# Kernel tuning notes

Hardware: AMD Instinct MI355X
Metric: run time of the kernel (lower is better)

## Reference

```python
import jax, jax.numpy as jnp
import numpy as np

N_STATES = 32
N_CAMP = 64
DAYS = 365
BATCH = 128
BASIS = 1e-10


def setup_inputs() -> dict:
    key = jax.random.key(0)
    k1, k2, k3 = jax.random.split(key, 3)
    S = N_STATES
    adstock = jax.random.uniform(k1, (BATCH, N_CAMP, DAYS), dtype=jnp.float32)
    mu = jax.random.uniform(k2, ((S - 1) * (S - 1),), dtype=jnp.float32)
    beta = jax.random.uniform(k3, (N_CAMP * (S - 1) * (S - 1),), dtype=jnp.float32)
    return {"adstock": adstock, "mu": mu, "beta": beta}


def _transition(adstock, mu, beta):
    # adstock: [B, C, D]; time T = D - 1 (first day dropped, as in adstock[:, :, 1:])
    S = N_STATES
    B, C, D = adstock.shape
    T = D - 1
    # call() passes -mu into make_transition_matrix
    mu_m = jnp.reshape(-mu, (1, 1, S - 1, S - 1))
    beta_m = jnp.reshape(beta, (C, S - 1, S - 1))
    # tensordot(adstock[b, :, 1:], beta, [0, 0]) for every b -> einsum over camp axis
    O_beta = jnp.einsum('bct,cij->btij', adstock[:, :, 1:], beta_m)  # [B,T,S-1,S-1]
    num = jnp.exp(O_beta + mu_m)
    den = 1.0 + jnp.sum(num, axis=-1, keepdims=True)
    Q_div = num / den                          # [B,T,S-1,S-1] off-diagonal probs
    Q_same = 1.0 - jnp.sum(Q_div, axis=-1)     # [B,T,S-1]    stay probability
    # The TF diag-set loop places, for row i of Q_div: columns j<i stay at j,
    # columns j>=i shift to j+1, and Q_same goes on column i (insert-diagonal).
    i = jnp.arange(S - 1)[:, None]             # [S-1,1]
    j = jnp.arange(S)[None, :]                 # [1,S]
    idx = jnp.clip(jnp.where(j < i, j, j - 1), 0, S - 2)  # [S-1,S]
    gathered = jnp.take_along_axis(Q_div, jnp.broadcast_to(idx, (B, T, S - 1, S)), axis=-1)
    Q_temp = jnp.where(j == i, Q_same[..., None], gathered)  # [B,T,S-1,S]
    # Absorbing last row: basis everywhere, mass 1-(S-1)*basis on last state.
    last = jnp.full((B, T, 1, S), BASIS, dtype=adstock.dtype)
    last = last.at[..., -1].set(1.0 - (S - 1) * BASIS)
    Q = jnp.concatenate([Q_temp, last], axis=2)  # [B,T,S,S]
    return jnp.maximum(Q, BASIS)


def reference(adstock, mu, beta):
    return _transition(adstock, mu, beta)
```

## Files before the change

### kernel.cpp

```cpp
#include <hip/hip_runtime.h>
#include <cstdint>
#include <cstddef>

#define Bb 128
#define Cc 64
#define Dd 365
#define Tt 364
#define Ss 32
#define SM1 31
#define NIJ 961
#define BASISF 1e-10f
#define NTILES 728
#define NBLK 256

typedef _Float16 f16x8 __attribute__((ext_vector_type(8)));
typedef _Float16 f16x4 __attribute__((ext_vector_type(4)));
typedef float f32x4 __attribute__((ext_vector_type(4)));

__global__ void prep_kernel(const float* __restrict__ mu,
                            const float* __restrict__ beta,
                            _Float16* __restrict__ B2,
                            float* __restrict__ emu_perm) {
    int idx = blockIdx.x * blockDim.x + threadIdx.x;
    int m = idx >> 6, c = idx & 63;
    int nq = m >> 8, rem = m & 255, qp = rem >> 6, p = (rem >> 4) & 3, v = rem & 15;
    int i = nq * 8 + qp * 2 + (v >> 3);
    int j = 4 * (v & 7) + p;
    float val = (i < SM1 && j < SM1) ? beta[c * NIJ + i * SM1 + j] : 0.0f;
    B2[((size_t)(c >> 3) * 1024 + m) * 8 + (c & 7)] = (_Float16)val;
    if (idx < 1024) {
        int m2 = idx;
        int nq2 = m2 >> 8, rem2 = m2 & 255, qp2 = rem2 >> 6;
        int p2 = (rem2 >> 4) & 3, v2 = rem2 & 15;
        int i2 = nq2 * 8 + qp2 * 2 + (v2 >> 3);
        int j2 = 4 * (v2 & 7) + p2;
        emu_perm[m2] = (i2 < SM1 && j2 < SM1) ? __expf(-mu[i2 * SM1 + j2]) : 1.0f;
    }
}

template <int CTRL>
__device__ __forceinline__ float dpp_mov(float x) {
    union { float f; int i; } u, v;
    u.f = x;
    v.i = __builtin_amdgcn_update_dpp(0, u.i, CTRL, 0xf, 0xf, true);
    return v.f;
}
template <int CTRL>
__device__ __forceinline__ float dpp_add(float s) { return s + dpp_mov<CTRL>(s); }

__global__ __launch_bounds__(1024, 1)
void transition_persist_kernel(const float* __restrict__ adstock,
                               const _Float16* __restrict__ B2,
                               const float* __restrict__ emu_perm,
                               float* __restrict__ out)
{
    const int tid  = threadIdx.x;
    const int lane = tid & 63;
    const int w    = tid >> 6;
    const int je   = lane & 15;
    const int grp  = lane >> 4;
    const int mh   = w >> 2;
    const int nq   = w & 3;
    const int a     = je & 7;
    const int ihalf = je >> 3;
    const int j0    = 4 * a;

    __shared__ _Float16 Blds[65536];
    __shared__ __align__(16) _Float16 Alds[64][72];

    #pragma unroll
    for (int s = 0; s < 8; ++s) {
        const int o8 = s * 8192 + tid * 8;
        *reinterpret_cast<f16x8*>(&Blds[o8]) =
            *reinterpret_cast<const f16x8*>(B2 + o8);
    }

    float emu[4][4];
    #pragma unroll
    for (int qp = 0; qp < 4; ++qp)
        #pragma unroll
        for (int p = 0; p < 4; ++p)
            emu[qp][p] = emu_perm[nq * 256 + qp * 64 + p * 16 + je];

    const float m3 = (a == 7) ? 0.0f : 1.0f;

    const int tb = (NTILES * blockIdx.x) / NBLK;
    const int te = (NTILES * (blockIdx.x + 1)) / NBLK;

    const int m_s = tid >> 4;
    const int c0  = (tid & 15) * 4;

    float av0, av1, av2, av3;
    {
        const int bt = tb * 64 + m_s;
        const int b = bt / Tt, t = bt - b * Tt;
        av0 = adstock[((size_t)b * Cc + c0 + 0) * Dd + 1 + t];
        av1 = adstock[((size_t)b * Cc + c0 + 1) * Dd + 1 + t];
        av2 = adstock[((size_t)b * Cc + c0 + 2) * Dd + 1 + t];
        av3 = adstock[((size_t)b * Cc + c0 + 3) * Dd + 1 + t];
    }

    for (int tile = tb; tile < te; ++tile) {
        __syncthreads();
        {
            f16x4 pk = {(_Float16)av0, (_Float16)av1, (_Float16)av2, (_Float16)av3};
            *reinterpret_cast<f16x4*>(&Alds[m_s][c0]) = pk;
        }
        __syncthreads();

        if (tile + 1 < te) {
            const int bt = (tile + 1) * 64 + m_s;
            const int b = bt / Tt, t = bt - b * Tt;
            av0 = adstock[((size_t)b * Cc + c0 + 0) * Dd + 1 + t];
            av1 = adstock[((size_t)b * Cc + c0 + 1) * Dd + 1 + t];
            av2 = adstock[((size_t)b * Cc + c0 + 2) * Dd + 1 + t];
            av3 = adstock[((size_t)b * Cc + c0 + 3) * Dd + 1 + t];
        }

        const f16x8 a0 = *reinterpret_cast<const f16x8*>(&Alds[mh * 16 + je][grp * 8]);
        const f16x8 a1 = *reinterpret_cast<const f16x8*>(&Alds[mh * 16 + je][32 + grp * 8]);

        const int bt0 = tile * 64 + mh * 16;

        #pragma unroll
        for (int qp = 0; qp < 4; ++qp) {
            const int colb = nq * 256 + qp * 64 + je;
            f16x8 Bf[8];
            #pragma unroll
            for (int p = 0; p < 4; ++p) {
                Bf[2 * p]     = *reinterpret_cast<const f16x8*>(
                    &Blds[((0 * 4 + grp) * 1024 + colb + p * 16) * 8]);
                Bf[2 * p + 1] = *reinterpret_cast<const f16x8*>(
                    &Blds[((1 * 4 + grp) * 1024 + colb + p * 16) * 8]);
            }

            f32x4 acc[4];
            #pragma unroll
            for (int p = 0; p < 4; ++p) {
                f32x4 z = {0.f, 0.f, 0.f, 0.f};
                f32x4 t0 = __builtin_amdgcn_mfma_f32_16x16x32_f16(a0, Bf[2 * p], z, 0, 0, 0);
                acc[p] = __builtin_amdgcn_mfma_f32_16x16x32_f16(a1, Bf[2 * p + 1], t0, 0, 0, 0);
            }

            const int i_lane = nq * 8 + 2 * qp + ihalf;
            const size_t obase = (size_t)(bt0 + grp * 4) * 1024
                               + (size_t)i_lane * 32 + j0;

            #pragma unroll
            for (int r = 0; r < 4; ++r) {
                float np[4];
                #pragma unroll
                for (int p = 0; p < 4; ++p) np[p] = __expf(acc[p][r]) * emu[qp][p];

                float s = np[0] + np[1] + fmaf(np[3], m3, np[2]);
                s = dpp_add<0xB1>(s);
                s = dpp_add<0x4E>(s);
                float t1 = dpp_mov<0x124>(s);
                float t2 = dpp_mov<0x12C>(s);
                s += (je & 4) ? t1 : t2;
                const float inv = __builtin_amdgcn_rcpf(1.0f + s);

                const float sh0 = dpp_mov<0x111>(np[3]);
                const float prev[4] = {sh0, np[0], np[1], np[2]};

                float v[4];
                #pragma unroll
                for (int p = 0; p < 4; ++p) {
                    const int j = j0 + p;
                    float x = (j < i_lane) ? np[p] * inv
                            : ((j == i_lane) ? inv : prev[p] * inv);
                    v[p] = fmaxf(x, BASISF);
                }
                if (nq == 3 && qp == 3) {
                    const bool ab = (i_lane == SM1);
                    v[0] = ab ? BASISF : v[0];
                    v[1] = ab ? BASISF : v[1];
                    v[2] = ab ? BASISF : v[2];
                    v[3] = ab ? ((a == 7) ? (1.0f - SM1 * BASISF) : BASISF) : v[3];
                }
                f32x4 vv = {v[0], v[1], v[2], v[3]};
                *reinterpret_cast<f32x4*>(out + obase + (size_t)r * 1024) = vv;
            }
        }
    }
}

__global__ __launch_bounds__(256, 4)
void transition_fallback_kernel(const float* __restrict__ adstock,
                                const float* __restrict__ beta,
                                const float* __restrict__ mu,
                                float* __restrict__ out) {
    const int b  = blockIdx.x;
    const int t0 = blockIdx.y * 16;
    const int tid = threadIdx.x;

    __shared__ float adT[Cc][16];
    __shared__ float num_lds[8][964];

    for (int k = tid; k < Cc * 16; k += 256) {
        int c = k >> 4, tt = k & 15, t = t0 + tt;
        adT[c][tt] = (t < Tt) ? adstock[(size_t)b * (Cc * Dd) + c * Dd + 1 + t] : 0.0f;
    }
    __syncthreads();

    const int ij0 = tid * 4;
    const bool active = (ij0 < 964);
    float acc[16][4];
    #pragma unroll
    for (int tt = 0; tt < 16; ++tt) { acc[tt][0]=0;acc[tt][1]=0;acc[tt][2]=0;acc[tt][3]=0; }

    if (active) {
        for (int c = 0; c < Cc; ++c) {
            const float* bsrc = beta + (size_t)c * NIJ;
            float w0 = (ij0+0<NIJ)?bsrc[ij0+0]:0.f, w1 = (ij0+1<NIJ)?bsrc[ij0+1]:0.f;
            float w2 = (ij0+2<NIJ)?bsrc[ij0+2]:0.f, w3 = (ij0+3<NIJ)?bsrc[ij0+3]:0.f;
            #pragma unroll
            for (int tt = 0; tt < 16; ++tt) {
                float av = adT[c][tt];
                acc[tt][0] = fmaf(av, w0, acc[tt][0]);
                acc[tt][1] = fmaf(av, w1, acc[tt][1]);
                acc[tt][2] = fmaf(av, w2, acc[tt][2]);
                acc[tt][3] = fmaf(av, w3, acc[tt][3]);
            }
        }
    }
    float m0=0,m1=0,m2=0,m3=0;
    if (active) {
        m0 = (ij0+0<NIJ)?mu[ij0+0]:0.f; m1 = (ij0+1<NIJ)?mu[ij0+1]:0.f;
        m2 = (ij0+2<NIJ)?mu[ij0+2]:0.f; m3 = (ij0+3<NIJ)?mu[ij0+3]:0.f;
    }
    const int q8 = tid >> 5, irow = tid & 31;
    #pragma unroll
    for (int half = 0; half < 2; ++half) {
        if (active) {
            #pragma unroll
            for (int q = 0; q < 8; ++q) {
                const int tt = half * 8 + q;
                num_lds[q][ij0+0] = __expf(acc[tt][0] - m0);
                num_lds[q][ij0+1] = __expf(acc[tt][1] - m1);
                num_lds[q][ij0+2] = __expf(acc[tt][2] - m2);
                num_lds[q][ij0+3] = __expf(acc[tt][3] - m3);
            }
        }
        __syncthreads();
        const int t = t0 + half * 8 + q8;
        if (t < Tt) {
            float* op = out + (((size_t)b * Tt + t) * Ss + irow) * Ss;
            if (irow < SM1) {
                float row[SM1]; float den = 1.0f;
                #pragma unroll
                for (int j = 0; j < SM1; ++j) { row[j] = num_lds[q8][irow*SM1+j]; den += row[j]; }
                const float inv = 1.0f / den;
                #pragma unroll
                for (int j = 0; j < Ss; ++j) {
                    float vv = (j < irow) ? row[j]*inv : ((j == irow) ? inv
                              : (j-1 < SM1 ? row[j-1]*inv : 0.f));
                    op[j] = fmaxf(vv, BASISF);
                }
            } else {
                #pragma unroll
                for (int j = 0; j < Ss; ++j) op[j] = (j == SM1) ? (1.0f - SM1*BASISF) : BASISF;
            }
        }
        __syncthreads();
    }
}

extern "C" void kernel_launch(void* const* d_in, const int* in_sizes, int n_in,
                              void* d_out, int out_size, void* d_ws, size_t ws_size,
                              hipStream_t stream) {
    const float* adstock = (const float*)d_in[0];
    const float* mu      = (const float*)d_in[1];
    const float* beta    = (const float*)d_in[2];
    float* out = (float*)d_out;

    const size_t need = (size_t)65536 * sizeof(_Float16) + 1024 * sizeof(float);

    if (ws_size >= need) {
        _Float16* B2 = (_Float16*)d_ws;
        float* emu_perm = (float*)((char*)d_ws + (size_t)65536 * sizeof(_Float16));
        prep_kernel<<<(1024 * Cc) / 256, 256, 0, stream>>>(mu, beta, B2, emu_perm);
        transition_persist_kernel<<<NBLK, 1024, 0, stream>>>(adstock, B2, emu_perm, out);
    } else {
        dim3 grid(Bb, (Tt + 15) / 16);
        transition_fallback_kernel<<<grid, 256, 0, stream>>>(adstock, beta, mu, out);
    }
}
```

Measured before the change: 43.56 us.

## Distribute per-wave work units and load A fragments directly from global memory

Replaces the block-level 64-row tile loop, which staged adstock through LDS with two __syncthreads per tile, with independent per-wave work units (16 rows × one i-quarter) split evenly across all waves. Each wave loads its own A fragment straight from global memory and converts it to fp16, which removes the block barriers and lets waves progress independently. The exp(-mu) factors move from registers into LDS to lower register pressure. The trade-off is that each adstock element is now loaded by four waves instead of once, and the global loads are strided with no prefetch overlap.

```diff
diff --git a/kernel.cpp b/kernel.cpp
--- a/kernel.cpp
+++ b/kernel.cpp
@@ -10,11 +10,11 @@
 #define SM1 31
 #define NIJ 961
 #define BASISF 1e-10f
-#define NTILES 728
 #define NBLK 256
+#define NUNITS 11648
+#define NWAVES 4096
 
 typedef _Float16 f16x8 __attribute__((ext_vector_type(8)));
-typedef _Float16 f16x4 __attribute__((ext_vector_type(4)));
 typedef float f32x4 __attribute__((ext_vector_type(4)));
 
 __global__ void prep_kernel(const float* __restrict__ mu,
@@ -23,17 +23,15 @@
                             float* __restrict__ emu_perm) {
     int idx = blockIdx.x * blockDim.x + threadIdx.x;
     int m = idx >> 6, c = idx & 63;
-    int nq = m >> 8, rem = m & 255, qp = rem >> 6, p = (rem >> 4) & 3, v = rem & 15;
-    int i = nq * 8 + qp * 2 + (v >> 3);
-    int j = 4 * (v & 7) + p;
+    int rem = m & 255;
+    int i = (m >> 8) * 8 + (rem >> 6) * 2 + ((rem & 15) >> 3);
+    int j = 4 * (rem & 7) + ((rem >> 4) & 3);
     float val = (i < SM1 && j < SM1) ? beta[c * NIJ + i * SM1 + j] : 0.0f;
     B2[((size_t)(c >> 3) * 1024 + m) * 8 + (c & 7)] = (_Float16)val;
     if (idx < 1024) {
-        int m2 = idx;
-        int nq2 = m2 >> 8, rem2 = m2 & 255, qp2 = rem2 >> 6;
-        int p2 = (rem2 >> 4) & 3, v2 = rem2 & 15;
-        int i2 = nq2 * 8 + qp2 * 2 + (v2 >> 3);
-        int j2 = 4 * (v2 & 7) + p2;
+        int m2 = idx, rem2 = m2 & 255;
+        int i2 = (m2 >> 8) * 8 + (rem2 >> 6) * 2 + ((rem2 & 15) >> 3);
+        int j2 = 4 * (rem2 & 7) + ((rem2 >> 4) & 3);
         emu_perm[m2] = (i2 < SM1 && j2 < SM1) ? __expf(-mu[i2 * SM1 + j2]) : 1.0f;
     }
 }
@@ -59,14 +57,12 @@
     const int w    = tid >> 6;
     const int je   = lane & 15;
     const int grp  = lane >> 4;
-    const int mh   = w >> 2;
-    const int nq   = w & 3;
     const int a     = je & 7;
     const int ihalf = je >> 3;
     const int j0    = 4 * a;
 
     __shared__ _Float16 Blds[65536];
-    __shared__ __align__(16) _Float16 Alds[64][72];
+    __shared__ float emuL[1024];
 
     #pragma unroll
     for (int s = 0; s < 8; ++s) {
@@ -74,53 +70,36 @@
         *reinterpret_cast<f16x8*>(&Blds[o8]) =
             *reinterpret_cast<const f16x8*>(B2 + o8);
     }
-
-    float emu[4][4];
-    #pragma unroll
-    for (int qp = 0; qp < 4; ++qp)
+    emuL[tid] = emu_perm[tid];
+    __syncthreads();
+
+    const float m3 = (a == 7) ? 0.0f : 1.0f;
+
+    const int gw = blockIdx.x * 16 + w;
+    const int ub = (int)(((long)NUNITS * gw) / NWAVES);
+    const int ue = (int)(((long)NUNITS * (gw + 1)) / NWAVES);
+
+    for (int u = ub; u < ue; ++u) {
+        const int chunk = u >> 2;
+        const int nq    = u & 3;
+        const int bt0   = chunk * 16;
+
+        const int bt = bt0 + je;
+        const int b  = bt / Tt, t = bt - b * Tt;
+        const float* abase = adstock + ((size_t)b * Cc) * Dd + 1 + t;
+
+        float a0f[8], a1f[8];
         #pragma unroll
-        for (int p = 0; p < 4; ++p)
-            emu[qp][p] = emu_perm[nq * 256 + qp * 64 + p * 16 + je];
-
-    const float m3 = (a == 7) ? 0.0f : 1.0f;
-
-    const int tb = (NTILES * blockIdx.x) / NBLK;
-    const int te = (NTILES * (blockIdx.x + 1)) / NBLK;
-
-    const int m_s = tid >> 4;
-    const int c0  = (tid & 15) * 4;
-
-    float av0, av1, av2, av3;
-    {
-        const int bt = tb * 64 + m_s;
-        const int b = bt / Tt, t = bt - b * Tt;
-        av0 = adstock[((size_t)b * Cc + c0 + 0) * Dd + 1 + t];
-        av1 = adstock[((size_t)b * Cc + c0 + 1) * Dd + 1 + t];
-        av2 = adstock[((size_t)b * Cc + c0 + 2) * Dd + 1 + t];
-        av3 = adstock[((size_t)b * Cc + c0 + 3) * Dd + 1 + t];
-    }
-
-    for (int tile = tb; tile < te; ++tile) {
-        __syncthreads();
-        {
-            f16x4 pk = {(_Float16)av0, (_Float16)av1, (_Float16)av2, (_Float16)av3};
-            *reinterpret_cast<f16x4*>(&Alds[m_s][c0]) = pk;
-        }
-        __syncthreads();
-
-        if (tile + 1 < te) {
-            const int bt = (tile + 1) * 64 + m_s;
-            const int b = bt / Tt, t = bt - b * Tt;
-            av0 = adstock[((size_t)b * Cc + c0 + 0) * Dd + 1 + t];
-            av1 = adstock[((size_t)b * Cc + c0 + 1) * Dd + 1 + t];
-            av2 = adstock[((size_t)b * Cc + c0 + 2) * Dd + 1 + t];
-            av3 = adstock[((size_t)b * Cc + c0 + 3) * Dd + 1 + t];
-        }
-
-        const f16x8 a0 = *reinterpret_cast<const f16x8*>(&Alds[mh * 16 + je][grp * 8]);
-        const f16x8 a1 = *reinterpret_cast<const f16x8*>(&Alds[mh * 16 + je][32 + grp * 8]);
-
-        const int bt0 = tile * 64 + mh * 16;
+        for (int u8 = 0; u8 < 8; ++u8) {
+            a0f[u8] = abase[(size_t)(grp * 8 + u8) * Dd];
+            a1f[u8] = abase[(size_t)(32 + grp * 8 + u8) * Dd];
+        }
+        f16x8 a0, a1;
+        #pragma unroll
+        for (int u8 = 0; u8 < 8; ++u8) {
+            a0[u8] = (_Float16)a0f[u8];
+            a1[u8] = (_Float16)a1f[u8];
+        }
 
         #pragma unroll
         for (int qp = 0; qp < 4; ++qp) {
@@ -134,6 +113,11 @@
                     &Blds[((1 * 4 + grp) * 1024 + colb + p * 16) * 8]);
             }
 
+            float emq[4];
+            #pragma unroll
+            for (int p = 0; p < 4; ++p)
+                emq[p] = emuL[nq * 256 + qp * 64 + p * 16 + je];
+
             f32x4 acc[4];
             #pragma unroll
             for (int p = 0; p < 4; ++p) {
@@ -150,7 +134,7 @@
             for (int r = 0; r < 4; ++r) {
                 float np[4];
                 #pragma unroll
-                for (int p = 0; p < 4; ++p) np[p] = __expf(acc[p][r]) * emu[qp][p];
+                for (int p = 0; p < 4; ++p) np[p] = __expf(acc[p][r]) * emq[p];
 
                 float s = np[0] + np[1] + fmaf(np[3], m3, np[2]);
                 s = dpp_add<0xB1>(s);
```

Result: slower. 48.35 us (+11.0%).

## Split output columns across block pairs with half-size B in LDS

Applied to the files above, without the earlier changes.

Each 1024-thread block becomes two 512-thread blocks. Each of the pair handles half of the output column groups (i rows) for the same time-tile slot and loads only half of the fp16 beta matrix into LDS. This halves per-block LDS and allows several blocks per CU, aiming for better occupancy and latency hiding than a single huge block. In exchange, each adstock tile is loaded and converted twice, once per column half.

```diff
diff --git a/kernel.cpp b/kernel.cpp
--- a/kernel.cpp
+++ b/kernel.cpp
@@ -10,8 +10,9 @@
 #define SM1 31
 #define NIJ 961
 #define BASISF 1e-10f
-#define NTILES 728
-#define NBLK 256
+#define NT64 728
+#define NSLOT 256
+#define NBLK2 512
 
 typedef _Float16 f16x8 __attribute__((ext_vector_type(8)));
 typedef _Float16 f16x4 __attribute__((ext_vector_type(4)));
@@ -23,17 +24,15 @@
                             float* __restrict__ emu_perm) {
     int idx = blockIdx.x * blockDim.x + threadIdx.x;
     int m = idx >> 6, c = idx & 63;
-    int nq = m >> 8, rem = m & 255, qp = rem >> 6, p = (rem >> 4) & 3, v = rem & 15;
-    int i = nq * 8 + qp * 2 + (v >> 3);
-    int j = 4 * (v & 7) + p;
+    int rem = m & 255;
+    int i = (m >> 8) * 8 + (rem >> 6) * 2 + ((rem & 15) >> 3);
+    int j = 4 * (rem & 7) + ((rem >> 4) & 3);
     float val = (i < SM1 && j < SM1) ? beta[c * NIJ + i * SM1 + j] : 0.0f;
     B2[((size_t)(c >> 3) * 1024 + m) * 8 + (c & 7)] = (_Float16)val;
     if (idx < 1024) {
-        int m2 = idx;
-        int nq2 = m2 >> 8, rem2 = m2 & 255, qp2 = rem2 >> 6;
-        int p2 = (rem2 >> 4) & 3, v2 = rem2 & 15;
-        int i2 = nq2 * 8 + qp2 * 2 + (v2 >> 3);
-        int j2 = 4 * (v2 & 7) + p2;
+        int m2 = idx, rem2 = m2 & 255;
+        int i2 = (m2 >> 8) * 8 + (rem2 >> 6) * 2 + ((rem2 & 15) >> 3);
+        int j2 = 4 * (rem2 & 7) + ((rem2 >> 4) & 3);
         emu_perm[m2] = (i2 < SM1 && j2 < SM1) ? __expf(-mu[i2 * SM1 + j2]) : 1.0f;
     }
 }
@@ -48,7 +47,7 @@
 template <int CTRL>
 __device__ __forceinline__ float dpp_add(float s) { return s + dpp_mov<CTRL>(s); }
 
-__global__ __launch_bounds__(1024, 1)
+__global__ __launch_bounds__(512, 4)
 void transition_persist_kernel(const float* __restrict__ adstock,
                                const _Float16* __restrict__ B2,
                                const float* __restrict__ emu_perm,
@@ -59,20 +58,25 @@
     const int w    = tid >> 6;
     const int je   = lane & 15;
     const int grp  = lane >> 4;
-    const int mh   = w >> 2;
-    const int nq   = w & 3;
+    const int mh   = w >> 1;
+    const int nqh  = w & 1;
     const int a     = je & 7;
     const int ihalf = je >> 3;
     const int j0    = 4 * a;
 
-    __shared__ _Float16 Blds[65536];
+    const int colhalf = blockIdx.x & 1;
+    const int slot    = blockIdx.x >> 1;
+    const int nqg     = colhalf * 2 + nqh;
+
+    __shared__ _Float16 Blds[32768];
     __shared__ __align__(16) _Float16 Alds[64][72];
 
     #pragma unroll
     for (int s = 0; s < 8; ++s) {
-        const int o8 = s * 8192 + tid * 8;
-        *reinterpret_cast<f16x8*>(&Blds[o8]) =
-            *reinterpret_cast<const f16x8*>(B2 + o8);
+        const int d8 = s * 4096 + tid * 8;
+        const int s8 = (s * 1024 + colhalf * 512) * 8 + tid * 8;
+        *reinterpret_cast<f16x8*>(&Blds[d8]) =
+            *reinterpret_cast<const f16x8*>(B2 + s8);
     }
 
     float emu[4][4];
@@ -80,41 +84,50 @@
     for (int qp = 0; qp < 4; ++qp)
         #pragma unroll
         for (int p = 0; p < 4; ++p)
-            emu[qp][p] = emu_perm[nq * 256 + qp * 64 + p * 16 + je];
+            emu[qp][p] = emu_perm[nqg * 256 + qp * 64 + p * 16 + je];
 
     const float m3 = (a == 7) ? 0.0f : 1.0f;
 
-    const int tb = (NTILES * blockIdx.x) / NBLK;
-    const int te = (NTILES * (blockIdx.x + 1)) / NBLK;
-
-    const int m_s = tid >> 4;
-    const int c0  = (tid & 15) * 4;
-
-    float av0, av1, av2, av3;
-    {
+    const int tb = (NT64 * slot) / NSLOT;
+    const int te = (NT64 * (slot + 1)) / NSLOT;
+
+    float av[2][4];
+    #pragma unroll
+    for (int s2 = 0; s2 < 2; ++s2) {
+        const int sl = tid + s2 * 512;
+        const int m_s = sl >> 4, c0 = (sl & 15) * 4;
         const int bt = tb * 64 + m_s;
         const int b = bt / Tt, t = bt - b * Tt;
-        av0 = adstock[((size_t)b * Cc + c0 + 0) * Dd + 1 + t];
-        av1 = adstock[((size_t)b * Cc + c0 + 1) * Dd + 1 + t];
-        av2 = adstock[((size_t)b * Cc + c0 + 2) * Dd + 1 + t];
-        av3 = adstock[((size_t)b * Cc + c0 + 3) * Dd + 1 + t];
+        av[s2][0] = adstock[((size_t)b * Cc + c0 + 0) * Dd + 1 + t];
+        av[s2][1] = adstock[((size_t)b * Cc + c0 + 1) * Dd + 1 + t];
+        av[s2][2] = adstock[((size_t)b * Cc + c0 + 2) * Dd + 1 + t];
+        av[s2][3] = adstock[((size_t)b * Cc + c0 + 3) * Dd + 1 + t];
     }
 
     for (int tile = tb; tile < te; ++tile) {
         __syncthreads();
-        {
-            f16x4 pk = {(_Float16)av0, (_Float16)av1, (_Float16)av2, (_Float16)av3};
+        #pragma unroll
+        for (int s2 = 0; s2 < 2; ++s2) {
+            const int sl = tid + s2 * 512;
+            const int m_s = sl >> 4, c0 = (sl & 15) * 4;
+            f16x4 pk = {(_Float16)av[s2][0], (_Float16)av[s2][1],
+                        (_Float16)av[s2][2], (_Float16)av[s2][3]};
             *reinterpret_cast<f16x4*>(&Alds[m_s][c0]) = pk;
         }
         __syncthreads();
 
         if (tile + 1 < te) {
-            const int bt = (tile + 1) * 64 + m_s;
-            const int b = bt / Tt, t = bt - b * Tt;
-            av0 = adstock[((size_t)b * Cc + c0 + 0) * Dd + 1 + t];
-            av1 = adstock[((size_t)b * Cc + c0 + 1) * Dd + 1 + t];
-            av2 = adstock[((size_t)b * Cc + c0 + 2) * Dd + 1 + t];
-            av3 = adstock[((size_t)b * Cc + c0 + 3) * Dd + 1 + t];
+            #pragma unroll
+            for (int s2 = 0; s2 < 2; ++s2) {
+                const int sl = tid + s2 * 512;
+                const int m_s = sl >> 4, c0 = (sl & 15) * 4;
+                const int bt = (tile + 1) * 64 + m_s;
+                const int b = bt / Tt, t = bt - b * Tt;
+                av[s2][0] = adstock[((size_t)b * Cc + c0 + 0) * Dd + 1 + t];
+                av[s2][1] = adstock[((size_t)b * Cc + c0 + 1) * Dd + 1 + t];
+                av[s2][2] = adstock[((size_t)b * Cc + c0 + 2) * Dd + 1 + t];
+                av[s2][3] = adstock[((size_t)b * Cc + c0 + 3) * Dd + 1 + t];
+            }
         }
 
         const f16x8 a0 = *reinterpret_cast<const f16x8*>(&Alds[mh * 16 + je][grp * 8]);
@@ -124,14 +137,14 @@
 
         #pragma unroll
         for (int qp = 0; qp < 4; ++qp) {
-            const int colb = nq * 256 + qp * 64 + je;
+            const int lcol = nqh * 256 + qp * 64 + je;
             f16x8 Bf[8];
             #pragma unroll
             for (int p = 0; p < 4; ++p) {
                 Bf[2 * p]     = *reinterpret_cast<const f16x8*>(
-                    &Blds[((0 * 4 + grp) * 1024 + colb + p * 16) * 8]);
+                    &Blds[((0 * 4 + grp) * 512 + lcol + p * 16) * 8]);
                 Bf[2 * p + 1] = *reinterpret_cast<const f16x8*>(
-                    &Blds[((1 * 4 + grp) * 1024 + colb + p * 16) * 8]);
+                    &Blds[((1 * 4 + grp) * 512 + lcol + p * 16) * 8]);
             }
 
             f32x4 acc[4];
@@ -142,7 +155,7 @@
                 acc[p] = __builtin_amdgcn_mfma_f32_16x16x32_f16(a1, Bf[2 * p + 1], t0, 0, 0, 0);
             }
 
-            const int i_lane = nq * 8 + 2 * qp + ihalf;
+            const int i_lane = nqg * 8 + 2 * qp + ihalf;
             const size_t obase = (size_t)(bt0 + grp * 4) * 1024
                                + (size_t)i_lane * 32 + j0;
 
@@ -171,7 +184,7 @@
                             : ((j == i_lane) ? inv : prev[p] * inv);
                     v[p] = fmaxf(x, BASISF);
                 }
-                if (nq == 3 && qp == 3) {
+                if (nqg == 3 && qp == 3) {
                     const bool ab = (i_lane == SM1);
                     v[0] = ab ? BASISF : v[0];
                     v[1] = ab ? BASISF : v[1];
@@ -280,7 +293,7 @@
         _Float16* B2 = (_Float16*)d_ws;
         float* emu_perm = (float*)((char*)d_ws + (size_t)65536 * sizeof(_Float16));
         prep_kernel<<<(1024 * Cc) / 256, 256, 0, stream>>>(mu, beta, B2, emu_perm);
-        transition_persist_kernel<<<NBLK, 1024, 0, stream>>>(adstock, B2, emu_perm, out);
+        transition_persist_kernel<<<NBLK2, 512, 0, stream>>>(adstock, B2, emu_perm, out);
     } else {
         dim3 grid(Bb, (Tt + 15) / 16);
         transition_fallback_kernel<<<grid, 256, 0, stream>>>(adstock, beta, mu, out);
```

New measurement: 46.93 us. 7.7% more time.
